# Kernel tuning notes

Hardware: AMD Instinct MI355X
Metric: run time of the kernel (lower is better)

The kernel has to match this reference:

```python
import jax, jax.numpy as jnp
import numpy as np

D_MODEL = 1024
N_SA = 8          # self-attention heads
N_RA = 8          # relational-attention heads
TOTAL = N_SA + N_RA
HEAD_DIM = D_MODEL // TOTAL   # 64
KEY_DIM = HEAD_DIM            # default key_dim = d_model // total_n_heads
N_REL = 8                     # n_relations (= n_heads_ra default)
REL_PROJ = KEY_DIM            # rel_proj_dim default
B, S = 4, 1024


def _rope(x, cos, sin):
    # x: [b, s, h, d]; cos/sin: [s, d//2]; interleaved-pair rotation as in apply_rotary_emb
    xr = x.reshape(x.shape[:-1] + (-1, 2))
    x_r, x_i = xr[..., 0], xr[..., 1]
    c = cos[None, :, None, :]
    s = sin[None, :, None, :]
    o_r = x_r * c - x_i * s
    o_i = x_r * s + x_i * c
    return jnp.stack([o_r, o_i], axis=-1).reshape(x.shape)


def setup_inputs() -> dict:
    key = jax.random.key(0)
    ks = jax.random.split(key, 16)
    def p(k, shape, scale=0.02):
        return jax.random.normal(k, shape, dtype=jnp.float32) * scale
    x = jax.random.normal(ks[0], (B, S, D_MODEL), dtype=jnp.float32)
    symbols = jax.random.normal(ks[1], (B, S, D_MODEL), dtype=jnp.float32)
    # standard RoPE frequency tables, shape [S, KEY_DIM//2]
    inv_freq = 1.0 / (10000.0 ** (np.arange(0, KEY_DIM, 2, dtype=np.float32) / KEY_DIM))
    ang = np.outer(np.arange(S, dtype=np.float32), inv_freq)
    freqs_cos = jnp.asarray(np.cos(ang), dtype=jnp.float32)
    freqs_sin = jnp.asarray(np.sin(ang), dtype=jnp.float32)
    return dict(
        x=x, symbols=symbols, freqs_cos=freqs_cos, freqs_sin=freqs_sin,
        # self-attention stream params
        wq_sa=p(ks[2], (D_MODEL, N_SA * KEY_DIM)),
        wk_sa=p(ks[3], (D_MODEL, N_SA * KEY_DIM)),
        wv_sa=p(ks[4], (D_MODEL, N_SA * HEAD_DIM)),
        wo_sa=p(ks[5], (N_SA * HEAD_DIM, N_SA * HEAD_DIM)),
        # relational-attention stream params
        wq_attn=p(ks[6], (D_MODEL, N_RA * KEY_DIM)),
        wk_attn=p(ks[7], (D_MODEL, N_RA * KEY_DIM)),
        wq_rel=p(ks[8], (D_MODEL, N_REL * REL_PROJ)),
        wk_rel=p(ks[9], (D_MODEL, N_REL * REL_PROJ)),
        wr=p(ks[10], (N_RA, HEAD_DIM, N_REL)),      # per-head relation->head_dim map
        wv_sym=p(ks[11], (D_MODEL, N_RA * HEAD_DIM)),  # symbol projection
        wo_ra=p(ks[12], (N_RA * HEAD_DIM, N_RA * HEAD_DIM)),
    )


def reference(x, symbols, freqs_cos, freqs_sin, wq_sa, wk_sa, wv_sa, wo_sa,
              wq_attn, wk_attn, wq_rel, wk_rel, wr, wv_sym, wo_ra):
    b, s, _ = x.shape
    attn_scale = 1.0 / jnp.sqrt(jnp.asarray(HEAD_DIM, dtype=x.dtype))
    rel_scale = 1.0 / jnp.sqrt(jnp.asarray(REL_PROJ, dtype=x.dtype))
    causal = jnp.tril(jnp.ones((s, s), dtype=bool))
    neg = jnp.where(causal, jnp.asarray(0.0, x.dtype), jnp.asarray(-jnp.inf, x.dtype))

    # ---- standard self-attention stream ----
    q = _rope((x @ wq_sa).reshape(b, s, N_SA, KEY_DIM), freqs_cos, freqs_sin)
    k = _rope((x @ wk_sa).reshape(b, s, N_SA, KEY_DIM), freqs_cos, freqs_sin)
    v = (x @ wv_sa).reshape(b, s, N_SA, HEAD_DIM)
    scores = jnp.einsum('bihd,bjhd->bhij', q, k) * attn_scale + neg
    attn = jax.nn.softmax(scores, axis=-1)
    sa_out = jnp.einsum('bhij,bjhd->bihd', attn, v).reshape(b, s, -1) @ wo_sa

    # ---- relational attention stream ----
    qa = _rope((x @ wq_attn).reshape(b, s, N_RA, KEY_DIM), freqs_cos, freqs_sin)
    ka = _rope((x @ wk_attn).reshape(b, s, N_RA, KEY_DIM), freqs_cos, freqs_sin)
    ra_scores = jnp.einsum('bihd,bjhd->bhij', qa, ka) * attn_scale + neg
    ra_attn = jax.nn.softmax(ra_scores, axis=-1)
    # relations r(i,j) in R^{n_rel}: inner products of relation projections, tanh-activated
    qr = (x @ wq_rel).reshape(b, s, N_REL, REL_PROJ)
    kr = (x @ wk_rel).reshape(b, s, N_REL, REL_PROJ)
    rel = jnp.tanh(jnp.einsum('bird,bjrd->bijr', qr, kr) * rel_scale)  # [b,s,s,n_rel]
    sv = (symbols @ wv_sym).reshape(b, s, N_RA, HEAD_DIM)
    sym_msg = jnp.einsum('bhij,bjhd->bihd', ra_attn, sv)
    rel_msg = jnp.einsum('bhij,bijr->bihr', ra_attn, rel)
    rel_proj = jnp.einsum('bihr,hdr->bihd', rel_msg, wr)
    ra_out = (sym_msg + rel_proj).reshape(b, s, -1) @ wo_ra

    # dual attention: concat the two streams along feature dim -> [b, s, d_model]
    return jnp.concatenate([sa_out, ra_out], axis=-1)
```

## Files before the change

### kernel.cpp

```cpp
#include <hip/hip_runtime.h>

typedef unsigned short u16;
typedef unsigned int u32;
typedef __attribute__((ext_vector_type(4))) short s16x4;
typedef __attribute__((ext_vector_type(8))) short s16x8;
typedef __attribute__((ext_vector_type(4))) float f32x4;

#define C_QSA 0
#define C_KSA 512
#define C_VSA 1024
#define C_QA  1536
#define C_KA  2048
#define C_QR  2560
#define C_KR  3072
#define C_SV  3584
#define LDP   4096

__device__ __forceinline__ u16 f2bf(float f) {
    union { float f; unsigned u; } v; v.f = f;
    return (u16)((v.u + 0x7FFFu + ((v.u >> 16) & 1u)) >> 16);
}
__device__ __forceinline__ float bf2f(u16 h) {
    union { unsigned u; float f; } v; v.u = ((unsigned)h) << 16; return v.f;
}
__device__ __forceinline__ float fexp(float y) {
    return __builtin_exp2f(y * 1.4426950408889634f);
}
__device__ __forceinline__ float ftanh(float x) {
    float e = __builtin_exp2f(x * 2.885390081777927f);
    return 1.f - 2.f / (e + 1.f);
}
__device__ __forceinline__ f32x4 mfma16(s16x8 a, s16x8 b, f32x4 c) {
    return __builtin_amdgcn_mfma_f32_16x16x32_bf16(a, b, c, 0, 0, 0);
}
__device__ __forceinline__ void gload16(const u16* g, u16* l) {
    __builtin_amdgcn_global_load_lds(
        (const __attribute__((address_space(1))) void*)g,
        (__attribute__((address_space(3))) void*)l, 16, 0, 0);
}


__global__ void cvt_f32_bf16(const float* __restrict__ in, u16* __restrict__ out, int n) {
    int i = (blockIdx.x * 256 + threadIdx.x) * 8;
    if (i >= n) return;
    float4 a = *(const float4*)(in + i);
    float4 b = *(const float4*)(in + i + 4);
    s16x8 o;
    o[0] = (short)f2bf(a.x); o[1] = (short)f2bf(a.y);
    o[2] = (short)f2bf(a.z); o[3] = (short)f2bf(a.w);
    o[4] = (short)f2bf(b.x); o[5] = (short)f2bf(b.y);
    o[6] = (short)f2bf(b.z); o[7] = (short)f2bf(b.w);
    *(s16x8*)(out + i) = o;
}

struct WP { const float* p[10]; };

__global__ void transpose_w(WP wp, u16* __restrict__ WcatT,
                            u16* __restrict__ woSaT, u16* __restrict__ woRaT) {
    const int z = blockIdx.z;
    const float* W;
    u16* Wt;
    int K;
    if (z < 8) { W = wp.p[z]; Wt = WcatT + (size_t)z * 524288; K = 1024; }
    else       { W = wp.p[z]; Wt = (z == 8) ? woSaT : woRaT;   K = 512;  }
    const int N = 512;
    const int kt = blockIdx.x * 32, nt = blockIdx.y * 32;
    if (kt >= K) return;
    __shared__ float t[32][33];
    const int c = threadIdx.x & 31, r0 = threadIdx.x >> 5;
#pragma unroll
    for (int it = 0; it < 4; ++it) {
        int r = it * 8 + r0;
        t[r][c] = W[(size_t)(kt + r) * N + nt + c];
    }
    __syncthreads();
#pragma unroll
    for (int it = 0; it < 4; ++it) {
        int r = it * 8 + r0;
        Wt[(size_t)(nt + r) * K + kt + c] = f2bf(t[c][r]);
    }
}

__global__ void transpose_v2(const u16* __restrict__ P, u16* __restrict__ Vt, int colOff) {
    const int st = blockIdx.x * 32, ht = blockIdx.y * 32, b = blockIdx.z;
    __shared__ u16 t[32][34];
    const int c = threadIdx.x & 31, r0 = threadIdx.x >> 5;
#pragma unroll
    for (int it = 0; it < 4; ++it) {
        int r = it * 8 + r0;
        t[r][c] = P[(size_t)(b * 1024 + st + r) * LDP + colOff + ht + c];
    }
    __syncthreads();
    const int cp = ((c & 15) >> 2) * 8 + (c >> 4) * 4 + (c & 3);
#pragma unroll
    for (int it = 0; it < 4; ++it) {
        int r = it * 8 + r0;
        Vt[(size_t)b * 524288 + (size_t)(ht + r) * 1024 + st + cp] = t[c][r];
    }
}


__global__ void rope_kernel(u16* __restrict__ P, const float* __restrict__ fcos,
                            const float* __restrict__ fsin) {
    int idx = blockIdx.x * 256 + threadIdx.x;
    int row = idx >> 10;
    int rem = idx & 1023;
    int region = rem >> 8;
    int pr = rem & 255;
    int head = pr >> 5, p = pr & 31;
    int off = (region + (region >> 1)) * 512;
    int col = off + head * 64 + 2 * p;
    int s = row & 1023;
    float c = fcos[s * 32 + p], sn = fsin[s * 32 + p];
    u32* ptr = (u32*)(P + (size_t)row * LDP + col);
    u32 v = *ptr;
    float xr = bf2f((u16)(v & 0xffff)), xi = bf2f((u16)(v >> 16));
    u16 o0 = f2bf(xr * c - xi * sn);
    u16 o1 = f2bf(xr * sn + xi * c);
    *ptr = (u32)o0 | ((u32)o1 << 16);
}


template<bool OUT_BF16>
__global__ __launch_bounds__(256) void gemm_bf16(
    const u16* __restrict__ A, const u16* __restrict__ A2, int lda, int nswitch,
    const u16* __restrict__ Bt, int ldb,
    void* __restrict__ Cp, int ldc, int ccolOff, int K)
{
    __shared__ u16 As[128][32];
    __shared__ u16 Bs[128][32];
    const int tid = threadIdx.x;
    const int m0 = blockIdx.x * 128, n0 = blockIdx.y * 128;
    const u16* Ause = (A2 != nullptr && n0 >= nswitch) ? A2 : A;
    const int w = tid >> 6, lane = tid & 63;
    const int w32 = w * 32;
    const int wm = (w >> 1) * 64, wn = (w & 1) * 64;
    const int lr = lane & 15, lg = lane >> 4;
    const int lrow = lane >> 2;
    const int lseg = (lane & 3) * 8;
    f32x4 acc[4][4] = {};

    for (int k0 = 0; k0 < K; k0 += 32) {
        const u16* ga = &Ause[(size_t)(m0 + w32 + lrow) * lda + k0 + lseg];
        const u16* gb = &Bt [(size_t)(n0 + w32 + lrow) * ldb + k0 + lseg];
        gload16(ga,            &As[w32][0]);
        gload16(ga + 16 * lda, &As[w32 + 16][0]);
        gload16(gb,            &Bs[w32][0]);
        gload16(gb + 16 * ldb, &Bs[w32 + 16][0]);
        __syncthreads();
        s16x8 af[4], bfr[4];
#pragma unroll
        for (int t = 0; t < 4; ++t) {
            af[t]  = *(const s16x8*)&As[wm + t * 16 + lr][lg * 8];
            bfr[t] = *(const s16x8*)&Bs[wn + t * 16 + lr][lg * 8];
        }
#pragma unroll
        for (int i = 0; i < 4; ++i)
#pragma unroll
            for (int j = 0; j < 4; ++j)
                acc[i][j] = mfma16(af[i], bfr[j], acc[i][j]);
        __syncthreads();
    }
#pragma unroll
    for (int i = 0; i < 4; ++i)
#pragma unroll
        for (int j = 0; j < 4; ++j)
#pragma unroll
            for (int r = 0; r < 4; ++r) {
                int row = m0 + wm + i * 16 + lg * 4 + r;
                int col = n0 + wn + j * 16 + lr;
                float val = acc[i][j][r];
                if (OUT_BF16)
                    ((u16*)Cp)[(size_t)row * ldc + ccolOff + col] = f2bf(val);
                else
                    ((float*)Cp)[(size_t)row * ldc + ccolOff + col] = val;
            }
}


__global__ __launch_bounds__(64) void attn_sa(u16* __restrict__ P, const u16* __restrict__ Vt) {
    const int bid = blockIdx.x;
    const int h = bid & 7;
    const int b = (bid >> 3) & 3;
    const int pr = bid >> 5;
    const int xt1 = pr, xt2 = 63 - pr;
    const int lane = threadIdx.x, lr = lane & 15, lg = lane >> 4;
    const size_t rowBase = (size_t)b * 1024;
    const int i0_1 = xt1 * 16, i0_2 = xt2 * 16;
    const int ir1 = i0_1 + lr, ir2 = i0_2 + lr;

    const u16* Kbase = P + rowBase * LDP + (C_KSA + h * 64);
    const u16* Vb = Vt + ((size_t)(b * 8 + h)) * 65536;

    s16x8 q1[2], q2[2];
    {
        const u16* q = P + (rowBase + ir1) * LDP + (C_QSA + h * 64) + lg * 8;
        q1[0] = *(const s16x8*)q; q1[1] = *(const s16x8*)(q + 32);
        q = P + (rowBase + ir2) * LDP + (C_QSA + h * 64) + lg * 8;
        q2[0] = *(const s16x8*)q; q2[1] = *(const s16x8*)(q + 32);
    }
    f32x4 o1[4] = {}, o2[4] = {};
    float l1 = 0.f, l2 = 0.f;
    const int njt  = (xt2 >> 1) + 1;
    const int njt1 = (xt1 >> 1) + 1;

    for (int jt = 0; jt < njt; ++jt) {
        const int j0 = jt * 32;
        const bool act1 = (jt < njt1);
        s16x8 kf[2][2], vfr[4];
#pragma unroll
        for (int sub = 0; sub < 2; ++sub) {
            const u16* kp = Kbase + (size_t)(j0 + sub * 16 + lr) * LDP + lg * 8;
            kf[sub][0] = *(const s16x8*)kp;
            kf[sub][1] = *(const s16x8*)(kp + 32);
        }
#pragma unroll
        for (int ds = 0; ds < 4; ++ds)
            vfr[ds] = *(const s16x8*)(Vb + (size_t)(ds * 16 + lr) * 1024 + j0 + 8 * lg);

        f32x4 sc2[2] = {{0.f,0.f,0.f,0.f},{0.f,0.f,0.f,0.f}};
        f32x4 sc1[2] = {{0.f,0.f,0.f,0.f},{0.f,0.f,0.f,0.f}};
#pragma unroll
        for (int sub = 0; sub < 2; ++sub) {
            sc2[sub] = mfma16(kf[sub][0], q2[0], sc2[sub]);
            sc2[sub] = mfma16(kf[sub][1], q2[1], sc2[sub]);
        }
        if (act1) {
#pragma unroll
            for (int sub = 0; sub < 2; ++sub) {
                sc1[sub] = mfma16(kf[sub][0], q1[0], sc1[sub]);
                sc1[sub] = mfma16(kf[sub][1], q1[1], sc1[sub]);
            }
        }
        s16x8 pa;
#pragma unroll
        for (int sub = 0; sub < 2; ++sub)
#pragma unroll
            for (int r = 0; r < 4; ++r) {
                int j = j0 + sub * 16 + 4 * lg + r;
                float p = (j <= ir2) ? fexp(sc2[sub][r] * 0.125f) : 0.f;
                l2 += p;
                pa[sub * 4 + r] = (short)f2bf(p);
            }
#pragma unroll
        for (int ds = 0; ds < 4; ++ds) o2[ds] = mfma16(pa, vfr[ds], o2[ds]);
        if (act1) {
#pragma unroll
            for (int sub = 0; sub < 2; ++sub)
#pragma unroll
                for (int r = 0; r < 4; ++r) {
                    int j = j0 + sub * 16 + 4 * lg + r;
                    float p = (j <= ir1) ? fexp(sc1[sub][r] * 0.125f) : 0.f;
                    l1 += p;
                    pa[sub * 4 + r] = (short)f2bf(p);
                }
#pragma unroll
            for (int ds = 0; ds < 4; ++ds) o1[ds] = mfma16(pa, vfr[ds], o1[ds]);
        }
    }
    l1 += __shfl_xor(l1, 16); l1 += __shfl_xor(l1, 32);
    l2 += __shfl_xor(l2, 16); l2 += __shfl_xor(l2, 32);
    float li1[4], li2[4];
#pragma unroll
    for (int r = 0; r < 4; ++r) {
        li1[r] = 1.f / __shfl(l1, 4 * lg + r);
        li2[r] = 1.f / __shfl(l2, 4 * lg + r);
    }
#pragma unroll
    for (int ds = 0; ds < 4; ++ds)
#pragma unroll
        for (int r = 0; r < 4; ++r) {
            P[(rowBase + i0_1 + 4 * lg + r) * LDP + (C_QSA + h * 64) + ds * 16 + lr] =
                f2bf(o1[ds][r] * li1[r]);
            P[(rowBase + i0_2 + 4 * lg + r) * LDP + (C_QSA + h * 64) + ds * 16 + lr] =
                f2bf(o2[ds][r] * li2[r]);
        }
}


__global__ __launch_bounds__(512) void attn_ra(u16* __restrict__ P, const u16* __restrict__ SVt,
                                               float* __restrict__ opart,
                                               float* __restrict__ mlr) {
    const int bid = blockIdx.x;
    const int slot = bid & 7;
    const int b = slot & 3, s = slot >> 2;
    const int xt = 63 - (bid >> 3);
    const int w = threadIdx.x >> 6, lane = threadIdx.x & 63;
    const int lr = lane & 15, lg = lane >> 4;
    const int h = w;
    const size_t rowBase = (size_t)b * 1024;
    const int i0 = xt * 16;
    const int ir = i0 + lr;

    __shared__ float relT[2][2][32][16][8];

    const u16* Kbase  = P + rowBase * LDP + (C_KA + h * 64);
    const u16* KRbase = P + rowBase * LDP + (C_KR + h * 64);
    const u16* Vb = SVt + ((size_t)(b * 8 + h)) * 65536;

    s16x8 qf[2], qrf[2];
    {
        const u16* q = P + (rowBase + ir) * LDP + (C_QA + h * 64) + lg * 8;
        qf[0] = *(const s16x8*)q; qf[1] = *(const s16x8*)(q + 32);
        const u16* qr = P + (rowBase + ir) * LDP + (C_QR + h * 64) + lg * 8;
        qrf[0] = *(const s16x8*)qr; qrf[1] = *(const s16x8*)(qr + 32);
    }
    f32x4 o[4] = {};
    float rmr[8] = {};
    float l = 0.f;
    const int njt = (xt >> 1) + 1;
    const int cnt = (njt - s + 1) >> 1;
    const int npair = (cnt + 1) >> 1;
    const int slotw = (w + lr) & 7;

    for (int u = 0; u < npair; ++u) {
        const int j0a = (s + 4 * u) * 32;
        const bool actB = (2 * u + 1) < cnt;
        const int j0b = actB ? j0a + 64 : j0a;
        s16x8 kfA[2][2], krA[2][2], kfB[2][2], krB[2][2], vfA[4], vfB[4];
#pragma unroll
        for (int sub = 0; sub < 2; ++sub) {
            const u16* kp = Kbase + (size_t)(j0a + sub * 16 + lr) * LDP + lg * 8;
            kfA[sub][0] = *(const s16x8*)kp;  kfA[sub][1] = *(const s16x8*)(kp + 32);
            const u16* krp = KRbase + (size_t)(j0a + sub * 16 + lr) * LDP + lg * 8;
            krA[sub][0] = *(const s16x8*)krp; krA[sub][1] = *(const s16x8*)(krp + 32);
            kp = Kbase + (size_t)(j0b + sub * 16 + lr) * LDP + lg * 8;
            kfB[sub][0] = *(const s16x8*)kp;  kfB[sub][1] = *(const s16x8*)(kp + 32);
            krp = KRbase + (size_t)(j0b + sub * 16 + lr) * LDP + lg * 8;
            krB[sub][0] = *(const s16x8*)krp; krB[sub][1] = *(const s16x8*)(krp + 32);
        }
#pragma unroll
        for (int ds = 0; ds < 4; ++ds) {
            vfA[ds] = *(const s16x8*)(Vb + (size_t)(ds * 16 + lr) * 1024 + j0a + 8 * lg);
            vfB[ds] = *(const s16x8*)(Vb + (size_t)(ds * 16 + lr) * 1024 + j0b + 8 * lg);
        }
        f32x4 scA[2] = {{0.f,0.f,0.f,0.f},{0.f,0.f,0.f,0.f}};
        f32x4 scB[2] = {{0.f,0.f,0.f,0.f},{0.f,0.f,0.f,0.f}};
        f32x4 rtA[2] = {{0.f,0.f,0.f,0.f},{0.f,0.f,0.f,0.f}};
        f32x4 rtB[2] = {{0.f,0.f,0.f,0.f},{0.f,0.f,0.f,0.f}};
#pragma unroll
        for (int sub = 0; sub < 2; ++sub) {
            scA[sub] = mfma16(kfA[sub][0], qf[0], scA[sub]);
            scA[sub] = mfma16(kfA[sub][1], qf[1], scA[sub]);
            rtA[sub] = mfma16(krA[sub][0], qrf[0], rtA[sub]);
            rtA[sub] = mfma16(krA[sub][1], qrf[1], rtA[sub]);
            scB[sub] = mfma16(kfB[sub][0], qf[0], scB[sub]);
            scB[sub] = mfma16(kfB[sub][1], qf[1], scB[sub]);
            rtB[sub] = mfma16(krB[sub][0], qrf[0], rtB[sub]);
            rtB[sub] = mfma16(krB[sub][1], qrf[1], rtB[sub]);
        }
        float pA[2][4], pB[2][4];
#pragma unroll
        for (int sub = 0; sub < 2; ++sub)
#pragma unroll
            for (int r = 0; r < 4; ++r) {
                int jA = j0a + sub * 16 + 4 * lg + r;
                int jB = j0b + sub * 16 + 4 * lg + r;
                pA[sub][r] = (jA <= ir) ? fexp(scA[sub][r] * 0.125f) : 0.f;
                pB[sub][r] = (actB && jB <= ir) ? fexp(scB[sub][r] * 0.125f) : 0.f;
                l += pA[sub][r] + pB[sub][r];
            }
#pragma unroll
        for (int sub = 0; sub < 2; ++sub)
#pragma unroll
            for (int r = 0; r < 4; ++r) {
                int jp = sub * 16 + 4 * lg + r;
                relT[u & 1][0][jp][lr][slotw] = ftanh(rtA[sub][r] * 0.125f);
                relT[u & 1][1][jp][lr][slotw] = ftanh(rtB[sub][r] * 0.125f);
            }
        __syncthreads();
#pragma unroll
        for (int sub = 0; sub < 2; ++sub)
#pragma unroll
            for (int r = 0; r < 4; ++r) {
                int jp = sub * 16 + 4 * lg + r;
                f32x4 a  = *(const f32x4*)&relT[u & 1][0][jp][lr][0];
                f32x4 bb = *(const f32x4*)&relT[u & 1][0][jp][lr][4];
                float pv = pA[sub][r];
#pragma unroll
                for (int k = 0; k < 4; ++k) {
                    rmr[k]     += pv * a[k];
                    rmr[4 + k] += pv * bb[k];
                }
                a  = *(const f32x4*)&relT[u & 1][1][jp][lr][0];
                bb = *(const f32x4*)&relT[u & 1][1][jp][lr][4];
                pv = pB[sub][r];
#pragma unroll
                for (int k = 0; k < 4; ++k) {
                    rmr[k]     += pv * a[k];
                    rmr[4 + k] += pv * bb[k];
                }
            }
        s16x8 paA, paB;
#pragma unroll
        for (int r = 0; r < 4; ++r) {
            paA[r]     = (short)f2bf(pA[0][r]);
            paA[4 + r] = (short)f2bf(pA[1][r]);
            paB[r]     = (short)f2bf(pB[0][r]);
            paB[4 + r] = (short)f2bf(pB[1][r]);
        }
#pragma unroll
        for (int ds = 0; ds < 4; ++ds) {
            o[ds] = mfma16(paA, vfA[ds], o[ds]);
            o[ds] = mfma16(paB, vfB[ds], o[ds]);
        }
    }

    l += __shfl_xor(l, 16); l += __shfl_xor(l, 32);
#pragma unroll
    for (int k = 0; k < 8; ++k) {
        float v = rmr[k];
        v += __shfl_xor(v, 16);
        v += __shfl_xor(v, 32);
        rmr[k] = v;
    }
    float g[8], t0[8];
    const int t = lr & 7;
#pragma unroll
    for (int k = 0; k < 8; ++k) g[k] = rmr[k];
#pragma unroll
    for (int k = 0; k < 8; ++k) t0[k] = (t & 1) ? g[(k + 1) & 7] : g[k];
#pragma unroll
    for (int k = 0; k < 8; ++k) g[k]  = (t & 2) ? t0[(k + 2) & 7] : t0[k];
#pragma unroll
    for (int k = 0; k < 8; ++k) t0[k] = (t & 4) ? g[(k + 4) & 7] : g[k];

    const int headRow = (b * 8 + h) * 1024;
#pragma unroll
    for (int ds = 0; ds < 4; ++ds)
#pragma unroll
        for (int r = 0; r < 4; ++r) {
            int row = headRow + i0 + 4 * lg + r;
            opart[((size_t)row * 2 + s) * 64 + ds * 16 + lr] = o[ds][r];
        }
    if (lg == 0) {
        float* pm = &mlr[((size_t)(headRow + i0 + lr) * 2 + s) * 10];
        pm[0] = l;
#pragma unroll
        for (int c = 0; c < 8; ++c) pm[1 + c] = t0[c];
    }
}


__global__ __launch_bounds__(256) void merge_ra(const float* __restrict__ opart,
                                                const float* __restrict__ mlr,
                                                const float* __restrict__ wr,
                                                u16* __restrict__ P) {
    const int gid = blockIdx.x * 4 + (threadIdx.x >> 6);
    const int d = threadIdx.x & 63;
    const int i = gid & 1023;
    const int h = (gid >> 10) & 7;
    const int b = gid >> 13;
    const float* ml0 = &mlr[(size_t)gid * 20];
    const float* ml1 = ml0 + 10;
    float ilt = 1.f / (ml0[0] + ml1[0]);
    float acc = (opart[(size_t)gid * 128 + d] +
                 opart[(size_t)gid * 128 + 64 + d]) * ilt;
#pragma unroll
    for (int c = 0; c < 8; ++c) {
        float rm = (ml0[1 + c] + ml1[1 + c]) * ilt;
        acc += rm * wr[h * 512 + d * 8 + c];
    }
    P[((size_t)(b * 1024 + i)) * LDP + C_QA + h * 64 + d] = f2bf(acc);
}


extern "C" void kernel_launch(void* const* d_in, const int* in_sizes, int n_in,
                              void* d_out, int out_size, void* d_ws, size_t ws_size,
                              hipStream_t stream)
{
    const float* x     = (const float*)d_in[0];
    const float* sym   = (const float*)d_in[1];
    const float* fcos  = (const float*)d_in[2];
    const float* fsin  = (const float*)d_in[3];
    const float* w_qsa = (const float*)d_in[4];
    const float* w_ksa = (const float*)d_in[5];
    const float* w_vsa = (const float*)d_in[6];
    const float* w_osa = (const float*)d_in[7];
    const float* w_qa  = (const float*)d_in[8];
    const float* w_ka  = (const float*)d_in[9];
    const float* w_qr  = (const float*)d_in[10];
    const float* w_kr  = (const float*)d_in[11];
    const float* wr    = (const float*)d_in[12];
    const float* w_sv  = (const float*)d_in[13];
    const float* w_ora = (const float*)d_in[14];

    char* ws = (char*)d_ws;
    u16* xb    = (u16*)(ws);
    u16* symb  = (u16*)(ws + (8u  << 20));
    u16* WcatT = (u16*)(ws + (16u << 20));
    u16* woSaT = (u16*)(ws + (24u << 20));
    u16* woRaT = (u16*)(ws + (24u << 20) + (512u << 10));
    u16* Pcat  = (u16*)(ws + (25u << 20));
    u16* vT    = (u16*)(ws + (57u << 20));
    u16* svT   = (u16*)(ws + (61u << 20));
    float* opart = (float*)(ws);
    float* mlrp  = (float*)(ws + (17u << 20));

    cvt_f32_bf16<<<2048, 256, 0, stream>>>(x,   xb,   4194304);
    cvt_f32_bf16<<<2048, 256, 0, stream>>>(sym, symb, 4194304);

    WP wp{{w_qsa, w_ksa, w_vsa, w_qa, w_ka, w_qr, w_kr, w_sv, w_osa, w_ora}};
    transpose_w<<<dim3(32, 16, 10), 256, 0, stream>>>(wp, WcatT, woSaT, woRaT);

    gemm_bf16<true><<<dim3(32, 32), 256, 0, stream>>>(
        xb, symb, 1024, C_SV, WcatT, 1024, Pcat, LDP, 0, 1024);

    rope_kernel<<<16384, 256, 0, stream>>>(Pcat, fcos, fsin);

    transpose_v2<<<dim3(32, 16, 4), 256, 0, stream>>>(Pcat, vT,  C_VSA);
    transpose_v2<<<dim3(32, 16, 4), 256, 0, stream>>>(Pcat, svT, C_SV);

    attn_sa<<<1024, 64, 0, stream>>>(Pcat, vT);
    attn_ra<<<512, 512, 0, stream>>>(Pcat, svT, opart, mlrp);
    merge_ra<<<8192, 256, 0, stream>>>(opart, mlrp, wr, Pcat);

    gemm_bf16<false><<<dim3(32, 8), 256, 0, stream>>>(
        Pcat + C_QSA, Pcat + C_QA, LDP, 512, woSaT, 512, d_out, 1024, 0, 512);
}
```

Measured before the change: 214.7 us.

## Double GEMM K-tile with XOR-swizzled LDS, remap blocks, merge bf16 conversions

The bf16 GEMM now stages a 64-wide K slice per iteration instead of 32, halving the barrier count. It uses an XOR column swizzle on LDS writes and reads to avoid bank conflicts. The projection GEMM gets a block-index remap that groups tiles for better L2 reuse of A and B. The two fp32->bf16 conversion launches are merged into one kernel. LDS use per block doubles, which may lower occupancy.

```diff
diff --git a/kernel.cpp b/kernel.cpp
--- a/kernel.cpp
+++ b/kernel.cpp
@@ -2,7 +2,6 @@
 
 typedef unsigned short u16;
 typedef unsigned int u32;
-typedef __attribute__((ext_vector_type(4))) short s16x4;
 typedef __attribute__((ext_vector_type(8))) short s16x8;
 typedef __attribute__((ext_vector_type(4))) float f32x4;
 
@@ -40,17 +39,21 @@
 }
 
 
-__global__ void cvt_f32_bf16(const float* __restrict__ in, u16* __restrict__ out, int n) {
+__global__ void cvt2_f32_bf16(const float* __restrict__ a, const float* __restrict__ b,
+                              u16* __restrict__ oa, u16* __restrict__ ob) {
     int i = (blockIdx.x * 256 + threadIdx.x) * 8;
-    if (i >= n) return;
-    float4 a = *(const float4*)(in + i);
-    float4 b = *(const float4*)(in + i + 4);
+    const int half = (i >= 4194304) ? 1 : 0;
+    const float* in = half ? b : a;
+    u16* out = half ? ob : oa;
+    int off = i - half * 4194304;
+    float4 x = *(const float4*)(in + off);
+    float4 y = *(const float4*)(in + off + 4);
     s16x8 o;
-    o[0] = (short)f2bf(a.x); o[1] = (short)f2bf(a.y);
-    o[2] = (short)f2bf(a.z); o[3] = (short)f2bf(a.w);
-    o[4] = (short)f2bf(b.x); o[5] = (short)f2bf(b.y);
-    o[6] = (short)f2bf(b.z); o[7] = (short)f2bf(b.w);
-    *(s16x8*)(out + i) = o;
+    o[0] = (short)f2bf(x.x); o[1] = (short)f2bf(x.y);
+    o[2] = (short)f2bf(x.z); o[3] = (short)f2bf(x.w);
+    o[4] = (short)f2bf(y.x); o[5] = (short)f2bf(y.y);
+    o[6] = (short)f2bf(y.z); o[7] = (short)f2bf(y.w);
+    *(s16x8*)(out + off) = o;
 }
 
 struct WP { const float* p[10]; };
@@ -121,44 +124,59 @@
 }
 
 
-template<bool OUT_BF16>
+template<bool OUT_BF16, bool SWZ>
 __global__ __launch_bounds__(256) void gemm_bf16(
     const u16* __restrict__ A, const u16* __restrict__ A2, int lda, int nswitch,
     const u16* __restrict__ Bt, int ldb,
     void* __restrict__ Cp, int ldc, int ccolOff, int K)
 {
-    __shared__ u16 As[128][32];
-    __shared__ u16 Bs[128][32];
+    __shared__ u16 As[128][64];
+    __shared__ u16 Bs[128][64];
     const int tid = threadIdx.x;
-    const int m0 = blockIdx.x * 128, n0 = blockIdx.y * 128;
+    int bx = blockIdx.x, by = blockIdx.y;
+    if (SWZ) {
+        int lin = by * gridDim.x + bx;
+        int k = lin & 7, j = lin >> 3;
+        bx = (k & 3) * 8 + (j & 7);
+        by = (k >> 2) * 16 + (j >> 3);
+    }
+    const int m0 = bx * 128, n0 = by * 128;
     const u16* Ause = (A2 != nullptr && n0 >= nswitch) ? A2 : A;
     const int w = tid >> 6, lane = tid & 63;
     const int w32 = w * 32;
     const int wm = (w >> 1) * 64, wn = (w & 1) * 64;
     const int lr = lane & 15, lg = lane >> 4;
-    const int lrow = lane >> 2;
-    const int lseg = (lane & 3) * 8;
+    const int srow = lane >> 3;
+    const int sc16 = ((lane & 7) ^ srow) * 8;
     f32x4 acc[4][4] = {};
 
-    for (int k0 = 0; k0 < K; k0 += 32) {
-        const u16* ga = &Ause[(size_t)(m0 + w32 + lrow) * lda + k0 + lseg];
-        const u16* gb = &Bt [(size_t)(n0 + w32 + lrow) * ldb + k0 + lseg];
+    for (int k0 = 0; k0 < K; k0 += 64) {
+        const u16* ga = &Ause[(size_t)(m0 + w32 + srow) * lda + k0 + sc16];
+        const u16* gb = &Bt [(size_t)(n0 + w32 + srow) * ldb + k0 + sc16];
         gload16(ga,            &As[w32][0]);
+        gload16(ga +  8 * lda, &As[w32 +  8][0]);
         gload16(ga + 16 * lda, &As[w32 + 16][0]);
+        gload16(ga + 24 * lda, &As[w32 + 24][0]);
         gload16(gb,            &Bs[w32][0]);
+        gload16(gb +  8 * ldb, &Bs[w32 +  8][0]);
         gload16(gb + 16 * ldb, &Bs[w32 + 16][0]);
+        gload16(gb + 24 * ldb, &Bs[w32 + 24][0]);
         __syncthreads();
-        s16x8 af[4], bfr[4];
-#pragma unroll
-        for (int t = 0; t < 4; ++t) {
-            af[t]  = *(const s16x8*)&As[wm + t * 16 + lr][lg * 8];
-            bfr[t] = *(const s16x8*)&Bs[wn + t * 16 + lr][lg * 8];
-        }
-#pragma unroll
-        for (int i = 0; i < 4; ++i)
-#pragma unroll
-            for (int j = 0; j < 4; ++j)
-                acc[i][j] = mfma16(af[i], bfr[j], acc[i][j]);
+#pragma unroll
+        for (int kk = 0; kk < 2; ++kk) {
+            s16x8 af[4], bfr[4];
+#pragma unroll
+            for (int t = 0; t < 4; ++t) {
+                const int ca = (((kk * 4 + lg) ^ (lr & 7)) * 8);
+                af[t]  = *(const s16x8*)&As[wm + t * 16 + lr][ca];
+                bfr[t] = *(const s16x8*)&Bs[wn + t * 16 + lr][ca];
+            }
+#pragma unroll
+            for (int i = 0; i < 4; ++i)
+#pragma unroll
+                for (int j = 0; j < 4; ++j)
+                    acc[i][j] = mfma16(af[i], bfr[j], acc[i][j]);
+        }
         __syncthreads();
     }
 #pragma unroll
@@ -497,13 +515,12 @@
     float* opart = (float*)(ws);
     float* mlrp  = (float*)(ws + (17u << 20));
 
-    cvt_f32_bf16<<<2048, 256, 0, stream>>>(x,   xb,   4194304);
-    cvt_f32_bf16<<<2048, 256, 0, stream>>>(sym, symb, 4194304);
+    cvt2_f32_bf16<<<4096, 256, 0, stream>>>(x, sym, xb, symb);
 
     WP wp{{w_qsa, w_ksa, w_vsa, w_qa, w_ka, w_qr, w_kr, w_sv, w_osa, w_ora}};
     transpose_w<<<dim3(32, 16, 10), 256, 0, stream>>>(wp, WcatT, woSaT, woRaT);
 
-    gemm_bf16<true><<<dim3(32, 32), 256, 0, stream>>>(
+    gemm_bf16<true, true><<<dim3(32, 32), 256, 0, stream>>>(
         xb, symb, 1024, C_SV, WcatT, 1024, Pcat, LDP, 0, 1024);
 
     rope_kernel<<<16384, 256, 0, stream>>>(Pcat, fcos, fsin);
@@ -515,6 +532,6 @@
     attn_ra<<<512, 512, 0, stream>>>(Pcat, svT, opart, mlrp);
     merge_ra<<<8192, 256, 0, stream>>>(opart, mlrp, wr, Pcat);
 
-    gemm_bf16<false><<<dim3(32, 8), 256, 0, stream>>>(
+    gemm_bf16<false, false><<<dim3(32, 8), 256, 0, stream>>>(
         Pcat + C_QSA, Pcat + C_QA, LDP, 512, woSaT, 512, d_out, 1024, 0, 512);
 }
```

Result: faster. 202.5 us (median of 2 runs) (-5.7%).
